# Performance work log

Measured on AMD Instinct MI355X. Metric: run time of the kernel, lower is better.

The kernel has to match this reference:

```python
import jax, jax.numpy as jnp
import numpy as np
from jax import lax

H = 1024          # Encoder_hidd == Decoder_hidd (fc consumes lstm1 output)
WIN_IN, WIN_OUT = 168, 24
B, F_IN = 256, 8
KEEP = 0.8        # 1 - dropout_probability(0.2)


def setup_inputs() -> dict:
    key = jax.random.key(0)
    ks = jax.random.split(key, 10)
    s = 1.0 / np.sqrt(H)
    return {
        "x":      jax.random.normal(ks[0], (B, WIN_IN + WIN_OUT, F_IN), jnp.float32),
        "conv_w": jax.random.normal(ks[1], (1, F_IN, 3), jnp.float32) * 0.2,  # [O,I,K]
        "conv_b": jnp.zeros((1,), jnp.float32),
        "Wih0":   jax.random.normal(ks[2], (4 * H, 1), jnp.float32) * s,
        "Whh0":   jax.random.normal(ks[3], (4 * H, H), jnp.float32) * s,
        "bih0":   jnp.zeros((4 * H,), jnp.float32),
        "bhh0":   jnp.zeros((4 * H,), jnp.float32),
        "Wih1":   jax.random.normal(ks[4], (4 * H, H), jnp.float32) * s,
        "Whh1":   jax.random.normal(ks[5], (4 * H, H), jnp.float32) * s,
        "bih1":   jnp.zeros((4 * H,), jnp.float32),
        "bhh1":   jnp.zeros((4 * H,), jnp.float32),
        "fc_w":   jax.random.normal(ks[6], (1, H), jnp.float32) * s,
        "fc_b":   jnp.zeros((1,), jnp.float32),
    }


def _forward(x, conv_w, conv_b, Wih0, Whh0, bih0, bhh0,
             Wih1, Whh1, bih1, bhh1, fc_w, fc_b):
    b0 = bih0 + bhh0
    b1 = bih1 + bhh1

    def cell(h0, c0, h1, c1, xt):
        # 2-layer LSTM cell, PyTorch gate order i, f, g, o
        g = xt @ Wih0.T + h0 @ Whh0.T + b0
        i, f, gg, o = jnp.split(g, 4, axis=-1)
        c0 = jax.nn.sigmoid(f) * c0 + jax.nn.sigmoid(i) * jnp.tanh(gg)
        h0 = jax.nn.sigmoid(o) * jnp.tanh(c0)
        g = h0 @ Wih1.T + h1 @ Whh1.T + b1
        i, f, gg, o = jnp.split(g, 4, axis=-1)
        c1 = jax.nn.sigmoid(f) * c1 + jax.nn.sigmoid(i) * jnp.tanh(gg)
        h1 = jax.nn.sigmoid(o) * jnp.tanh(c1)
        return h0, c0, h1, c1

    # ---- CNN front-end on encoder window ----
    xe = jnp.transpose(x[:, :WIN_IN, :], (0, 2, 1))            # [B, F_IN, 168]
    y = lax.conv_general_dilated(xe, conv_w, (1,), [(1, 1)],
                                 dimension_numbers=("NCH", "OIH", "NCH"))
    y = jax.nn.relu(y + conv_b[None, :, None])                 # [B, 1, 168]
    y = lax.reduce_window(y, -jnp.inf, lax.max,
                          (1, 1, 2), (1, 1, 2), "VALID")      # [B, 1, 84]
    seq = jnp.transpose(y, (2, 0, 1))                           # [84, B, 1]

    bsz = x.shape[0]
    z = jnp.zeros((bsz, H), x.dtype)

    def enc_step(carry, xt):
        return cell(*carry, xt), None

    carry, _ = lax.scan(enc_step, (z, z, z, z), seq)            # t=0 LSTM pass
    h1_last = carry[2]

    dkey = jax.random.key(42)

    def dropout(v, t):
        m = jax.random.bernoulli(jax.random.fold_in(dkey, t), KEEP, v.shape)
        return jnp.where(m, v / KEEP, jnp.zeros((), v.dtype))

    def fc(v):
        return v @ fc_w.T + fc_b

    y0 = fc(dropout(h1_last, 0))                                # [B, 1]

    def dec_step(carry, t):
        h0, c0, h1, c1, yp = carry
        h0, c0, h1, c1 = cell(h0, c0, h1, c1, yp)               # feed y_pred back
        yt = fc(dropout(h1, t))
        return (h0, c0, h1, c1, yt), yt

    _, ys = lax.scan(dec_step, (*carry, y0), jnp.arange(1, WIN_OUT))
    ys = jnp.swapaxes(ys, 0, 1)[..., 0]                         # [B, 23]
    return jnp.concatenate([y0, ys], axis=1)                    # [B, 24]


def reference(x, conv_w, conv_b, Wih0, Whh0, bih0, bhh0,
              Wih1, Whh1, bih1, bhh1, fc_w, fc_b):
    return _forward(x, conv_w, conv_b, Wih0, Whh0, bih0, bhh0,
                    Wih1, Whh1, bih1, bhh1, fc_w, fc_b)
```

## Files before the change

kernel.cpp:

```cpp
#include <hip/hip_runtime.h>
#include <stdint.h>

typedef _Float16 f16;
typedef f16  f16x8 __attribute__((ext_vector_type(8)));
typedef float f32x4 __attribute__((ext_vector_type(4)));
typedef unsigned u32x4 __attribute__((ext_vector_type(4)));

#define H0_OFF    0u
#define H1_OFF    2097152u
#define WHH0F_OFF 4194304u
#define SEQ_OFF   12582912u
#define YACC_OFF  12668928u
#define FLAG_OFF  12693504u

__device__ __forceinline__ unsigned rotl32(unsigned x, int d){ return (x<<d)|(x>>(32-d)); }

__device__ __forceinline__ uint2 tf2x32(unsigned k0, unsigned k1, unsigned x0, unsigned x1){
  unsigned kx = k0 ^ k1 ^ 0x1BD11BDAu;
  x0 += k0; x1 += k1;
#define TFR(r) { x0 += x1; x1 = rotl32(x1,(r)); x1 ^= x0; }
  TFR(13) TFR(15) TFR(26) TFR(6)  x0 += k1; x1 += kx + 1u;
  TFR(17) TFR(29) TFR(16) TFR(24) x0 += kx; x1 += k0 + 2u;
  TFR(13) TFR(15) TFR(26) TFR(6)  x0 += k0; x1 += k1 + 3u;
  TFR(17) TFR(29) TFR(16) TFR(24) x0 += k1; x1 += kx + 4u;
  TFR(13) TFR(15) TFR(26) TFR(6)  x0 += kx; x1 += k0 + 5u;
#undef TFR
  return make_uint2(x0, x1);
}

__device__ __forceinline__ bool drop_keep(uint2 fk, unsigned n){
  uint2 o = tf2x32(fk.x, fk.y, 0u, n);
  unsigned bits = o.x ^ o.y;
  float u = __uint_as_float((bits >> 9) | 0x3f800000u) - 1.0f;
  return u < 0.8f;
}

__device__ __forceinline__ float sigf(float x){ return 1.0f/(1.0f + __expf(-x)); }
__device__ __forceinline__ float thf(float x){ return 1.0f - 2.0f/(__expf(2.0f*x) + 1.0f); }

__device__ __forceinline__ void st_dword_sc(void* p, unsigned v){
  asm volatile("global_store_dword %0, %1, off sc0 sc1" :: "v"(p), "v"(v) : "memory");
}
__device__ __forceinline__ void st_dwordx4_sc(void* p, u32x4 v){
  asm volatile("global_store_dwordx4 %0, %1, off sc0 sc1" :: "v"(p), "v"(v) : "memory");
}
__device__ __forceinline__ unsigned ld_dword_sc(const void* p){
  unsigned r;
  asm volatile("global_load_dword %0, %1, off sc0 sc1\n\ts_waitcnt vmcnt(0)"
               : "=v"(r) : "v"(p) : "memory");
  return r;
}

__device__ __forceinline__ void gbar(unsigned* flagsH, unsigned e,
                                     int tid, int lblk, bool inv){
  asm volatile("s_waitcnt vmcnt(0)" ::: "memory");
  __syncthreads();
  if (tid == 0) st_dword_sc(flagsH + lblk*32, e);
  if (inv) __builtin_amdgcn_fence(__ATOMIC_ACQUIRE, "agent");
  if (tid < 128){
    unsigned* f = flagsH + tid*32;
    while (ld_dword_sc(f) < e) __builtin_amdgcn_s_sleep(1);
  }
  __syncthreads();
  __builtin_amdgcn_sched_barrier(0);
}

__global__ void k_init(uint4* __restrict__ hz, uint4* __restrict__ yz, uint4* __restrict__ fz){
  unsigned i = blockIdx.x*256u + threadIdx.x;
  if (i < 262144u){ hz[i] = uint4{0,0,0,0}; }
  else if (i < 263680u){ yz[i - 262144u] = uint4{0,0,0,0}; }
  else if (i < 265728u){ fz[i - 263680u] = uint4{0,0,0,0}; }
}

__global__ void k_seq(const float* __restrict__ x, const float* __restrict__ cw,
                      const float* __restrict__ cb, float* __restrict__ seq){
  const int q = blockIdx.x;
  const int b = threadIdx.x;
  float best = -1e30f;
#pragma unroll
  for (int ssub = 0; ssub < 2; ++ssub){
    int p = 2*q + ssub;
    float acc = cb[0];
#pragma unroll
    for (int k = 0; k < 3; ++k){
      int t = p - 1 + k;
      if (t >= 0 && t < 168){
        const float* xp = x + ((size_t)b*192 + t)*8;
#pragma unroll
        for (int i = 0; i < 8; ++i) acc = fmaf(xp[i], cw[i*3 + k], acc);
      }
    }
    acc  = fmaxf(acc, 0.0f);
    best = fmaxf(best, acc);
  }
  seq[(q<<8) + b] = best;
}

__global__ void __launch_bounds__(512) k_wpack(const float* __restrict__ W, f16* __restrict__ dst){
  const int hgrp = blockIdx.x;
  const int tid = threadIdx.x;
  const int l   = tid & 63;
  const int w   = tid >> 6;
  const int j0  = hgrp << 3;
#pragma unroll
  for (int fi = 0; fi < 8; ++fi){
    const int f = (w << 3) + fi;
    const int c = f >> 1, T = f & 1;
    const int r = l & 15;
    const int u = (T << 2) + (r >> 2);
    const int g = r & 3;
    const float* src = W + (((size_t)((g << 10) + j0 + u)) << 10) + (c << 5) + ((l >> 4) << 3);
    float4 a = *(const float4*)src;
    float4 b = *(const float4*)(src + 4);
    f16x8 v;
    v[0]=(f16)a.x; v[1]=(f16)a.y; v[2]=(f16)a.z; v[3]=(f16)a.w;
    v[4]=(f16)b.x; v[5]=(f16)b.y; v[6]=(f16)b.z; v[7]=(f16)b.w;
    *(f16x8*)(dst + ((size_t)hgrp << 15) + (f << 9) + (l << 3)) = v;
  }
}

#define MFMA16(a,b,c) __builtin_amdgcn_mfma_f32_16x16x32_f16((a),(b),(c),0,0,0)

__global__ void __launch_bounds__(512, 1) k_main(
    const float* __restrict__ Wih0, const float* __restrict__ Whh0,
    const float* __restrict__ bih0, const float* __restrict__ bhh0,
    const float* __restrict__ Wih1, const float* __restrict__ Whh1,
    const float* __restrict__ bih1, const float* __restrict__ bhh1,
    const float* __restrict__ fc_w, const float* __restrict__ fc_b,
    char* __restrict__ ws, float* __restrict__ out)
{
  extern __shared__ char smem_[];
  f16* lds = (f16*)smem_;
  f16* stage  = lds + 65536;
  f16* wstage = lds + 66560;

  const int tid  = threadIdx.x;
  const int blk  = blockIdx.x;
  const int hgrp = blk & 127;
  const int bgrp = blk >> 7;
  const int j0   = hgrp << 3;
  const int l    = tid & 63;
  const int w8   = tid >> 6;
  const int q    = l >> 4;
  const int c16  = l & 15;
  const int lcol = (w8 << 4) + c16;
  const int bcol = (bgrp << 7) + lcol;

  {
    const float* srcs[2] = {Wih1, Whh1};
#pragma unroll
    for (int m = 0; m < 2; ++m){
#pragma unroll
      for (int fi = 0; fi < 8; ++fi){
        const int f = (w8 << 3) + fi;
        const int c = f >> 1, T = f & 1;
        const int r = c16;
        const int uu = (T << 2) + (r >> 2);
        const int g = r & 3;
        const float* src = srcs[m] + (((size_t)((g << 10) + j0 + uu)) << 10) + (c << 5) + (q << 3);
        float4 a = *(const float4*)src;
        float4 b = *(const float4*)(src + 4);
        f16x8 v;
        v[0]=(f16)a.x; v[1]=(f16)a.y; v[2]=(f16)a.z; v[3]=(f16)a.w;
        v[4]=(f16)b.x; v[5]=(f16)b.y; v[6]=(f16)b.z; v[7]=(f16)b.w;
        *(f16x8*)(lds + m*32768 + (f << 9) + (l << 3)) = v;
      }
    }
  }
  __syncthreads();

  float bias0t[2][4], bias1t[2][4], wi0t[2][4];
#pragma unroll
  for (int t = 0; t < 2; ++t){
    const int uu = j0 + q + t*4;
#pragma unroll
    for (int g = 0; g < 4; ++g){
      int row = (g << 10) + uu;
      bias0t[t][g] = bih0[row] + bhh0[row];
      bias1t[t][g] = bih1[row] + bhh1[row];
      wi0t[t][g]   = Wih0[row];
    }
  }
  const float fcw0 = fc_w[j0 + q] * 1.25f;
  const float fcw1 = fc_w[j0 + q + 4] * 1.25f;
  const float fcb  = fc_b[0];

  const int base_h = (q << 11) + (bcol << 3);

  f16* H0 = (f16*)(ws + H0_OFF);
  f16* H1 = (f16*)(ws + H1_OFF);
  const f16* whh0f = (const f16*)(ws + WHH0F_OFF) + ((size_t)hgrp << 15);
  const float* seq = (const float*)(ws + SEQ_OFF);
  float* y_acc = (float*)(ws + YACC_OFF);
  unsigned* flagsH = (unsigned*)(ws + FLAG_OFF) + bgrp*4096;

  u32x4 wreg[8];
#pragma unroll
  for (int ch = 0; ch < 8; ++ch)
    wreg[ch] = *(const u32x4*)(whh0f + ((size_t)ch << 12) + (tid << 3));

  float c0[2] = {0,0}, c1[2] = {0,0};
  unsigned ep = 0;

  {
    float xb = seq[bcol];
#pragma unroll
    for (int t = 0; t < 2; ++t){
      float pi = bias0t[t][0] + wi0t[t][0]*xb;
      float pf = bias0t[t][1] + wi0t[t][1]*xb;
      float pg = bias0t[t][2] + wi0t[t][2]*xb;
      float po = bias0t[t][3] + wi0t[t][3]*xb;
      c0[t] = sigf(pi)*thf(pg);
      float h0n = sigf(po)*thf(c0[t]);
      stage[(lcol << 3) + q + t*4] = (f16)h0n;
    }
  }
  __syncthreads();
  if (tid < 128){
    u32x4 v = ((const u32x4*)stage)[tid];
    st_dwordx4_sc((char*)(H0 + 262144 + (hgrp << 11) + (bgrp << 10)) + tid*16, v);
  }
  ++ep; gbar(flagsH, ep, tid, hgrp, true);

#pragma unroll 1
  for (int s = 0; s < 107; ++s){
    const int p = s & 1;
    const bool doA = (s < 106);
    const f16* hb0 = H0 + (p^1)*262144 + base_h;
    const f16* hb1 = H1 + p*262144 + base_h;

    f16x8 X0[2][4], X1[2][4];
    f32x4 accB0 = (f32x4){0,0,0,0}, accB1 = (f32x4){0,0,0,0};
    f32x4 accA0 = (f32x4){0,0,0,0}, accA1 = (f32x4){0,0,0,0};
#define LDX(B, CB) { _Pragma("unroll") for (int i = 0; i < 4; ++i){ const int c = (CB)+i; \
      X0[B][i] = *(const f16x8*)(hb0 + c*8192); \
      X1[B][i] = *(const f16x8*)(hb1 + c*8192); } }
#define MMW(B, CH) { const f16* wsb = wstage + (((CH)&1) << 12) + (l << 3); \
      _Pragma("unroll") for (int i = 0; i < 4; ++i){ \
      f16x8 wf0 = *(const f16x8*)(wsb + ((2*i  ) << 9)); \
      f16x8 wf1 = *(const f16x8*)(wsb + ((2*i+1) << 9)); \
      accA0 = MFMA16(wf0, X0[B][i], accA0); \
      accA1 = MFMA16(wf1, X0[B][i], accA1); } }
#define MMB(B, CB) { _Pragma("unroll") for (int i = 0; i < 4; ++i){ const int c = (CB)+i; \
      f16x8 wa0 = *(const f16x8*)(lds + ((2*c  ) << 9) + (l << 3)); \
      f16x8 wa1 = *(const f16x8*)(lds + ((2*c+1) << 9) + (l << 3)); \
      f16x8 wb0 = *(const f16x8*)(lds + 32768 + ((2*c  ) << 9) + (l << 3)); \
      f16x8 wb1 = *(const f16x8*)(lds + 32768 + ((2*c+1) << 9) + (l << 3)); \
      accB0 = MFMA16(wa0, X0[B][i], accB0); \
      accB0 = MFMA16(wb0, X1[B][i], accB0); \
      accB1 = MFMA16(wa1, X0[B][i], accB1); \
      accB1 = MFMA16(wb1, X1[B][i], accB1); } }
    LDX(0, 0) LDX(1, 4)
    *(u32x4*)(wstage + (tid << 3)) = wreg[0];
    __syncthreads();
#pragma unroll
    for (int ch = 0; ch < 8; ++ch){
      if (ch < 7) *(u32x4*)(wstage + (((ch+1)&1) << 12) + (tid << 3)) = wreg[ch+1];
      if (doA) MMW(ch&1, ch)
      MMB(ch&1, ch*4)
      if (ch < 6) LDX(ch&1, (ch+2)*4)
      if (ch < 7) __syncthreads();
    }
#undef LDX
#undef MMW
#undef MMB

    float h1n[2];
    {
      f32x4 at[2] = {accB0, accB1};
#pragma unroll
      for (int t = 0; t < 2; ++t){
        float pi = at[t][0] + bias1t[t][0];
        float pf = at[t][1] + bias1t[t][1];
        float pg = at[t][2] + bias1t[t][2];
        float po = at[t][3] + bias1t[t][3];
        c1[t]  = sigf(pf)*c1[t] + sigf(pi)*thf(pg);
        h1n[t] = sigf(po)*thf(c1[t]);
        stage[(lcol << 3) + q + t*4] = (f16)h1n[t];
      }
    }
    __syncthreads();
    if (tid < 128){
      u32x4 v = ((const u32x4*)stage)[tid];
      st_dwordx4_sc((char*)(H1 + (p^1)*262144 + (hgrp << 11) + (bgrp << 10)) + tid*16, v);
    }

    if (s >= 83){
      const int tau = s - 83;
      uint2 fk = tf2x32(0u, 42u, 0u, (unsigned)tau);
      unsigned n0 = ((unsigned)bcol << 10) + (unsigned)(j0 + q);
      unsigned n1 = n0 + 4u;
      float v = (drop_keep(fk, n0) ? h1n[0]*fcw0 : 0.f)
              + (drop_keep(fk, n1) ? h1n[1]*fcw1 : 0.f);
      v += __shfl_xor(v, 16, 64);
      v += __shfl_xor(v, 32, 64);
      if (q == 0) atomicAdd(y_acc + (tau << 8) + bcol, v);
      ++ep; gbar(flagsH, ep, tid, hgrp, false);
    } else {
      __syncthreads();
    }

    if (doA){
      const int s1 = s + 1;
      float xb;
      if (s1 < 84){
        xb = seq[(s1 << 8) + bcol];
      } else {
        const int tp = s1 - 84;
        float yp = fcb + __uint_as_float(ld_dword_sc(y_acc + (tp << 8) + bcol));
        if (hgrp == 0 && q == 0) out[bcol*24 + tp] = yp;
        xb = yp;
      }
      f32x4 at[2] = {accA0, accA1};
#pragma unroll
      for (int t = 0; t < 2; ++t){
        float pi = at[t][0] + bias0t[t][0] + wi0t[t][0]*xb;
        float pf = at[t][1] + bias0t[t][1] + wi0t[t][1]*xb;
        float pg = at[t][2] + bias0t[t][2] + wi0t[t][2]*xb;
        float po = at[t][3] + bias0t[t][3] + wi0t[t][3]*xb;
        c0[t]  = sigf(pf)*c0[t] + sigf(pi)*thf(pg);
        float h0n = sigf(po)*thf(c0[t]);
        stage[(lcol << 3) + q + t*4] = (f16)h0n;
      }
      __syncthreads();
      if (tid < 128){
        u32x4 v = ((const u32x4*)stage)[tid];
        st_dwordx4_sc((char*)(H0 + p*262144 + (hgrp << 11) + (bgrp << 10)) + tid*16, v);
      }
      ++ep; gbar(flagsH, ep, tid, hgrp, true);
    }
  }

  if (hgrp == 0 && q == 0)
    out[bcol*24 + 23] = fcb + __uint_as_float(ld_dword_sc(y_acc + (23 << 8) + bcol));
}

extern "C" void kernel_launch(void* const* d_in, const int* in_sizes, int n_in,
                              void* d_out, int out_size, void* d_ws, size_t ws_size,
                              hipStream_t stream)
{
  const float* x    = (const float*)d_in[0];
  const float* cw   = (const float*)d_in[1];
  const float* cb   = (const float*)d_in[2];
  const float* Wih0 = (const float*)d_in[3];
  const float* Whh0 = (const float*)d_in[4];
  const float* bih0 = (const float*)d_in[5];
  const float* bhh0 = (const float*)d_in[6];
  const float* Wih1 = (const float*)d_in[7];
  const float* Whh1 = (const float*)d_in[8];
  const float* bih1 = (const float*)d_in[9];
  const float* bhh1 = (const float*)d_in[10];
  const float* fc_w = (const float*)d_in[11];
  const float* fc_b = (const float*)d_in[12];
  float* out = (float*)d_out;
  char*  ws  = (char*)d_ws;

  hipLaunchKernelGGL(k_init, dim3(1040), dim3(256), 0, stream,
                     (uint4*)(ws + H0_OFF), (uint4*)(ws + YACC_OFF), (uint4*)(ws + FLAG_OFF));
  hipLaunchKernelGGL(k_seq,  dim3(84), dim3(256), 0, stream, x, cw, cb, (float*)(ws + SEQ_OFF));
  hipLaunchKernelGGL(k_wpack, dim3(128), dim3(512), 0, stream, Whh0, (f16*)(ws + WHH0F_OFF));
  hipLaunchKernelGGL(k_main, dim3(256), dim3(512), 149504, stream,
                     Wih0, Whh0, bih0, bhh0, Wih1, Whh1, bih1, bhh1,
                     fc_w, fc_b, ws, out);
}
```

Measured before the change: 2.681 ms.

## Fuse Whh0 packing into main kernel and spread fc atomics over slots

Drops the separate weight-packing kernel: each block now converts its own slice of Whh0 from fp32 to fp16 directly into registers. The y accumulator is split into 8 slots chosen by hgrp&7, so atomicAdds from the 128 hidden groups contend less, and readers issue 8 loads asynchronously and sum them. The workspace is also shrunk, which reduces the zero-init work. In exchange, k_main start-up does strided fp32 global reads, and each feedback read issues 8 loads instead of one.

```diff
diff --git a/kernel.cpp b/kernel.cpp
--- a/kernel.cpp
+++ b/kernel.cpp
@@ -7,11 +7,10 @@
 typedef unsigned u32x4 __attribute__((ext_vector_type(4)));
 
 #define H0_OFF    0u
-#define H1_OFF    2097152u
-#define WHH0F_OFF 4194304u
-#define SEQ_OFF   12582912u
-#define YACC_OFF  12668928u
-#define FLAG_OFF  12693504u
+#define H1_OFF    1048576u
+#define YSLOT_OFF 2097152u
+#define SEQ_OFF   2293760u
+#define FLAG_OFF  2379776u
 
 __device__ __forceinline__ unsigned rotl32(unsigned x, int d){ return (x<<d)|(x>>(32-d)); }
 
@@ -50,6 +49,9 @@
                : "=v"(r) : "v"(p) : "memory");
   return r;
 }
+__device__ __forceinline__ void ld_sc_async(unsigned& d, const void* p){
+  asm volatile("global_load_dword %0, %1, off sc0 sc1" : "=&v"(d) : "v"(p));
+}
 
 __device__ __forceinline__ void gbar(unsigned* flagsH, unsigned e,
                                      int tid, int lblk, bool inv){
@@ -67,9 +69,9 @@
 
 __global__ void k_init(uint4* __restrict__ hz, uint4* __restrict__ yz, uint4* __restrict__ fz){
   unsigned i = blockIdx.x*256u + threadIdx.x;
-  if (i < 262144u){ hz[i] = uint4{0,0,0,0}; }
-  else if (i < 263680u){ yz[i - 262144u] = uint4{0,0,0,0}; }
-  else if (i < 265728u){ fz[i - 263680u] = uint4{0,0,0,0}; }
+  if (i < 32768u){ hz[i] = uint4{0,0,0,0}; }
+  else if (i < 45056u){ yz[i - 32768u] = uint4{0,0,0,0}; }
+  else if (i < 47104u){ fz[i - 45056u] = uint4{0,0,0,0}; }
 }
 
 __global__ void k_seq(const float* __restrict__ x, const float* __restrict__ cw,
@@ -94,29 +96,6 @@
     best = fmaxf(best, acc);
   }
   seq[(q<<8) + b] = best;
-}
-
-__global__ void __launch_bounds__(512) k_wpack(const float* __restrict__ W, f16* __restrict__ dst){
-  const int hgrp = blockIdx.x;
-  const int tid = threadIdx.x;
-  const int l   = tid & 63;
-  const int w   = tid >> 6;
-  const int j0  = hgrp << 3;
-#pragma unroll
-  for (int fi = 0; fi < 8; ++fi){
-    const int f = (w << 3) + fi;
-    const int c = f >> 1, T = f & 1;
-    const int r = l & 15;
-    const int u = (T << 2) + (r >> 2);
-    const int g = r & 3;
-    const float* src = W + (((size_t)((g << 10) + j0 + u)) << 10) + (c << 5) + ((l >> 4) << 3);
-    float4 a = *(const float4*)src;
-    float4 b = *(const float4*)(src + 4);
-    f16x8 v;
-    v[0]=(f16)a.x; v[1]=(f16)a.y; v[2]=(f16)a.z; v[3]=(f16)a.w;
-    v[4]=(f16)b.x; v[5]=(f16)b.y; v[6]=(f16)b.z; v[7]=(f16)b.w;
-    *(f16x8*)(dst + ((size_t)hgrp << 15) + (f << 9) + (l << 3)) = v;
-  }
 }
 
 #define MFMA16(a,b,c) __builtin_amdgcn_mfma_f32_16x16x32_f16((a),(b),(c),0,0,0)
@@ -169,6 +148,22 @@
   }
   __syncthreads();
 
+  u32x4 wreg[8];
+#pragma unroll
+  for (int ch = 0; ch < 8; ++ch){
+    const int f = (ch << 3) + w8;
+    const int c = f >> 1, T = f & 1;
+    const int uu = (T << 2) + (c16 >> 2);
+    const int g = c16 & 3;
+    const float* src = Whh0 + (((size_t)((g << 10) + j0 + uu)) << 10) + (c << 5) + (q << 3);
+    float4 a = *(const float4*)src;
+    float4 b = *(const float4*)(src + 4);
+    f16x8 v;
+    v[0]=(f16)a.x; v[1]=(f16)a.y; v[2]=(f16)a.z; v[3]=(f16)a.w;
+    v[4]=(f16)b.x; v[5]=(f16)b.y; v[6]=(f16)b.z; v[7]=(f16)b.w;
+    wreg[ch] = __builtin_bit_cast(u32x4, v);
+  }
+
   float bias0t[2][4], bias1t[2][4], wi0t[2][4];
 #pragma unroll
   for (int t = 0; t < 2; ++t){
@@ -189,15 +184,9 @@
 
   f16* H0 = (f16*)(ws + H0_OFF);
   f16* H1 = (f16*)(ws + H1_OFF);
-  const f16* whh0f = (const f16*)(ws + WHH0F_OFF) + ((size_t)hgrp << 15);
   const float* seq = (const float*)(ws + SEQ_OFF);
-  float* y_acc = (float*)(ws + YACC_OFF);
+  float* y_slot = (float*)(ws + YSLOT_OFF);
   unsigned* flagsH = (unsigned*)(ws + FLAG_OFF) + bgrp*4096;
-
-  u32x4 wreg[8];
-#pragma unroll
-  for (int ch = 0; ch < 8; ++ch)
-    wreg[ch] = *(const u32x4*)(whh0f + ((size_t)ch << 12) + (tid << 3));
 
   float c0[2] = {0,0}, c1[2] = {0,0};
   unsigned ep = 0;
@@ -294,7 +283,7 @@
               + (drop_keep(fk, n1) ? h1n[1]*fcw1 : 0.f);
       v += __shfl_xor(v, 16, 64);
       v += __shfl_xor(v, 32, 64);
-      if (q == 0) atomicAdd(y_acc + (tau << 8) + bcol, v);
+      if (q == 0) atomicAdd(y_slot + ((hgrp & 7)*24 + tau)*256 + bcol, v);
       ++ep; gbar(flagsH, ep, tid, hgrp, false);
     } else {
       __syncthreads();
@@ -307,7 +296,15 @@
         xb = seq[(s1 << 8) + bcol];
       } else {
         const int tp = s1 - 84;
-        float yp = fcb + __uint_as_float(ld_dword_sc(y_acc + (tp << 8) + bcol));
+        const float* yb = y_slot + tp*256 + bcol;
+        unsigned r[8];
+#pragma unroll
+        for (int m = 0; m < 8; ++m) ld_sc_async(r[m], yb + m*6144);
+        asm volatile("s_waitcnt vmcnt(0)" ::: "memory");
+        __builtin_amdgcn_sched_barrier(0);
+        float yp = fcb;
+#pragma unroll
+        for (int m = 0; m < 8; ++m) yp += __uint_as_float(r[m]);
         if (hgrp == 0 && q == 0) out[bcol*24 + tp] = yp;
         xb = yp;
       }
@@ -331,8 +328,18 @@
     }
   }
 
-  if (hgrp == 0 && q == 0)
-    out[bcol*24 + 23] = fcb + __uint_as_float(ld_dword_sc(y_acc + (23 << 8) + bcol));
+  if (hgrp == 0 && q == 0){
+    const float* yb = y_slot + 23*256 + bcol;
+    unsigned r[8];
+#pragma unroll
+    for (int m = 0; m < 8; ++m) ld_sc_async(r[m], yb + m*6144);
+    asm volatile("s_waitcnt vmcnt(0)" ::: "memory");
+    __builtin_amdgcn_sched_barrier(0);
+    float yp = fcb;
+#pragma unroll
+    for (int m = 0; m < 8; ++m) yp += __uint_as_float(r[m]);
+    out[bcol*24 + 23] = yp;
+  }
 }
 
 extern "C" void kernel_launch(void* const* d_in, const int* in_sizes, int n_in,
@@ -355,10 +362,9 @@
   float* out = (float*)d_out;
   char*  ws  = (char*)d_ws;
 
-  hipLaunchKernelGGL(k_init, dim3(1040), dim3(256), 0, stream,
-                     (uint4*)(ws + H0_OFF), (uint4*)(ws + YACC_OFF), (uint4*)(ws + FLAG_OFF));
+  hipLaunchKernelGGL(k_init, dim3(184), dim3(256), 0, stream,
+                     (uint4*)(ws + H1_OFF), (uint4*)(ws + YSLOT_OFF), (uint4*)(ws + FLAG_OFF));
   hipLaunchKernelGGL(k_seq,  dim3(84), dim3(256), 0, stream, x, cw, cb, (float*)(ws + SEQ_OFF));
-  hipLaunchKernelGGL(k_wpack, dim3(128), dim3(512), 0, stream, Whh0, (f16*)(ws + WHH0F_OFF));
   hipLaunchKernelGGL(k_main, dim3(256), dim3(512), 149504, stream,
                      Wih0, Whh0, bih0, bhh0, Wih1, Whh1, bih1, bhh1,
                      fc_w, fc_b, ws, out);
```

Result: faster. 2.623 ms (-2.2%).
